# Kernel optimization log

Hardware: AMD Instinct MI355X
Metric: run time of the kernel (lower is better)

Reference implementation:

```python
import jax, jax.numpy as jnp
import numpy as np

B, N, IN_DIM, D = 32, 2000, 3, 5
GROUP = 5
TOPK = 110

def setup_inputs() -> dict:
    key = jax.random.key(0)
    ks = jax.random.split(key, 11)
    def lin(k, fan_in, fan_out):
        kw, kb = jax.random.split(k)
        bound = 1.0 / np.sqrt(fan_in)
        W = jax.random.uniform(kw, (fan_in, fan_out), jnp.float32, -bound, bound)
        b = jax.random.uniform(kb, (fan_out,), jnp.float32, -bound, bound)
        return W, b
    Wi, bi = lin(ks[1], IN_DIM, D)
    Wq, bq = lin(ks[2], D, D)
    Wk, bk = lin(ks[3], D, D)
    Wv, bv = lin(ks[4], D, D)
    Wo, bo = lin(ks[5], D, D)
    in_mat = jax.random.normal(ks[0], (B, N, IN_DIM), jnp.float32)
    return {"in_mat": in_mat, "Wi": Wi, "bi": bi, "Wq": Wq, "bq": bq,
            "Wk": Wk, "bk": bk, "Wv": Wv, "bv": bv, "Wo": Wo, "bo": bo}

def reference(in_mat, Wi, bi, Wq, bq, Wk, bk, Wv, bv, Wo, bo):
    # input projection: [B,N,3] -> [B,N,D]
    x = in_mat @ Wi + bi
    Q = x @ Wq + bq
    K = x @ Wk + bk
    V = x @ Wv + bv
    scores = jnp.einsum('bnd,bmd->bnm', Q, K) / jnp.sqrt(jnp.float32(D))  # [B,N,N]
    attn = jax.nn.softmax(scores, axis=-1)
    context = jnp.einsum('bnm,bmd->bnd', attn, V)
    _out = context @ Wo + bo  # transformed output (unused downstream, as in source)

    # select_points, fully batched
    diag = jnp.diagonal(attn, axis1=1, axis2=2)               # [B,N]
    attn_sums = diag.reshape(B, N // GROUP, GROUP).sum(-1)    # [B, N/5]
    max_group_idx = jnp.argmax(attn_sums, axis=1)             # [B]
    grp_idx = max_group_idx[:, None] * GROUP + jnp.arange(GROUP)[None, :]  # [B,5]
    group_points = jnp.take_along_axis(in_mat, grp_idx[:, :, None], axis=1)  # [B,5,3]
    centroid = group_points.mean(axis=1)                       # [B,3]
    distances = jnp.linalg.norm(in_mat - centroid[:, None, :], axis=-1)  # [B,N]
    _, closest = jax.lax.top_k(-distances, TOPK)               # smallest distances, [B,110]
    selected = jnp.take_along_axis(in_mat, closest[:, :, None], axis=1)  # [B,110,3]
    return selected
```

## Files before the change

### kernel.cpp

```cpp
#include <hip/hip_runtime.h>
#include <stdint.h>

#define BB      32
#define NN      2000
#define TOPK_   110
#define NBIN    2048

__device__ __forceinline__ void fold_weights(
    const float* __restrict__ Wi, const float* __restrict__ bi,
    const float* __restrict__ Wq, const float* __restrict__ bq,
    const float* __restrict__ Wk, const float* __restrict__ bk,
    float Gp[3][3], float vp[3])
{
    const float pf = 0.44721359549995793f * 1.4426950408889634f;
    float Mq[15], Mk[15], cq[5];
#pragma unroll
    for (int d = 0; d < 5; ++d) {
        float s = bq[d];
#pragma unroll
        for (int k = 0; k < 5; ++k) s += bi[k] * Wq[k * 5 + d];
        cq[d] = s;
    }
#pragma unroll
    for (int i = 0; i < 3; ++i)
#pragma unroll
        for (int d = 0; d < 5; ++d) {
            float sq = 0.f, sk = 0.f;
#pragma unroll
            for (int k = 0; k < 5; ++k) {
                sq += Wi[i * 5 + k] * Wq[k * 5 + d];
                sk += Wi[i * 5 + k] * Wk[k * 5 + d];
            }
            Mq[i * 5 + d] = sq;
            Mk[i * 5 + d] = sk;
        }
#pragma unroll
    for (int i = 0; i < 3; ++i)
#pragma unroll
        for (int j = 0; j < 3; ++j) {
            float s = 0.f;
#pragma unroll
            for (int d = 0; d < 5; ++d) s += Mq[i * 5 + d] * Mk[j * 5 + d];
            Gp[i][j] = s * pf;
        }
#pragma unroll
    for (int j = 0; j < 3; ++j) {
        float s = 0.f;
#pragma unroll
        for (int d = 0; d < 5; ++d) s += cq[d] * Mk[j * 5 + d];
        vp[j] = s * pf;
    }
}

__global__ __launch_bounds__(1024) void k_diag(
    const float* __restrict__ in_mat,
    const float* __restrict__ Wi, const float* __restrict__ bi,
    const float* __restrict__ Wq, const float* __restrict__ bq,
    const float* __restrict__ Wk, const float* __restrict__ bk,
    float* __restrict__ diag)
{
    __shared__ float partial[16][128];

    const int b   = blockIdx.y;
    const int rc  = blockIdx.x;
    const int t   = threadIdx.x;
    const int wid = t >> 6;
    const int lane = t & 63;
    const float* inb = in_mat + (size_t)b * NN * 3;

    float Gp[3][3], vp[3];
    fold_weights(Wi, bi, Wq, bq, Wk, bk, Gp, vp);

    float h[2][3];
#pragma unroll
    for (int r = 0; r < 2; ++r) {
        const int row = rc * 128 + r * 64 + lane;
        float p0 = 0.f, p1 = 0.f, p2 = 0.f;
        if (row < NN) {
            p0 = inb[row * 3 + 0];
            p1 = inb[row * 3 + 1];
            p2 = inb[row * 3 + 2];
        }
#pragma unroll
        for (int j = 0; j < 3; ++j)
            h[r][j] = p0 * Gp[0][j] + p1 * Gp[1][j] + p2 * Gp[2][j] + vp[j];
    }

    float acc0 = 0.f, acc1 = 0.f;
    const int m0 = wid * 125;
#pragma unroll 5
    for (int m = m0; m < m0 + 125; ++m) {
        const float px = inb[m * 3 + 0];
        const float py = inb[m * 3 + 1];
        const float pz = inb[m * 3 + 2];
        const float e0 = fmaf(h[0][0], px, fmaf(h[0][1], py, h[0][2] * pz));
        const float e1 = fmaf(h[1][0], px, fmaf(h[1][1], py, h[1][2] * pz));
        acc0 += __builtin_amdgcn_exp2f(e0);
        acc1 += __builtin_amdgcn_exp2f(e1);
    }
    partial[wid][lane]      = acc0;
    partial[wid][64 + lane] = acc1;
    __syncthreads();

    if (t < 128) {
        const int row = rc * 128 + t;
        if (row < NN) {
            float sum = partial[0][t];
#pragma unroll
            for (int w = 1; w < 16; ++w) sum += partial[w][t];
            const float p0 = inb[row * 3 + 0];
            const float p1 = inb[row * 3 + 1];
            const float p2 = inb[row * 3 + 2];
            float hh[3];
#pragma unroll
            for (int j = 0; j < 3; ++j)
                hh[j] = p0 * Gp[0][j] + p1 * Gp[1][j] + p2 * Gp[2][j] + vp[j];
            const float e = fmaf(hh[0], p0, fmaf(hh[1], p1, hh[2] * p2));
            diag[(size_t)b * NN + row] = __builtin_amdgcn_exp2f(e) / sum;
        }
    }
}

__global__ __launch_bounds__(1024) void k_select(
    const float* __restrict__ in_mat,
    const float* __restrict__ diag,
    float* __restrict__ out)
{
    __shared__ unsigned long long keys[2048];
    __shared__ unsigned long long cand[2048];
    __shared__ unsigned int hist[NBIN];
    __shared__ unsigned int sA[NBIN];
    __shared__ unsigned int sB[NBIN];
    __shared__ float        wv[16];
    __shared__ int          wi_[16];
    __shared__ float        centroid[3];
    __shared__ int          thrBin, cnt;

    const int b = blockIdx.x;
    const int t = threadIdx.x;
    const float* dg  = diag + (size_t)b * NN;
    const float* inb = in_mat + (size_t)b * NN * 3;

    hist[t] = 0u; hist[t + 1024] = 0u;
    if (t == 0) cnt = 0;

    float v = -INFINITY; int idx = 0x7fffffff;
    if (t < NN / 5) {
        float s = dg[t * 5 + 0];
        s += dg[t * 5 + 1];
        s += dg[t * 5 + 2];
        s += dg[t * 5 + 3];
        s += dg[t * 5 + 4];
        v = s; idx = t;
    }
#pragma unroll
    for (int off = 32; off > 0; off >>= 1) {
        const float ov = __shfl_down(v, off);
        const int   oi = __shfl_down(idx, off);
        if (ov > v || (ov == v && oi < idx)) { v = ov; idx = oi; }
    }
    if ((t & 63) == 0) { wv[t >> 6] = v; wi_[t >> 6] = idx; }
    __syncthreads();

    if (t == 0) {
        float bv = wv[0]; int bidx = wi_[0];
#pragma unroll
        for (int w = 1; w < 16; ++w) {
            if (wv[w] > bv || (wv[w] == bv && wi_[w] < bidx)) {
                bv = wv[w]; bidx = wi_[w];
            }
        }
        const int base = bidx * 5;
#pragma unroll
        for (int d = 0; d < 3; ++d) {
            float s = inb[(base + 0) * 3 + d];
            s = __fadd_rn(s, inb[(base + 1) * 3 + d]);
            s = __fadd_rn(s, inb[(base + 2) * 3 + d]);
            s = __fadd_rn(s, inb[(base + 3) * 3 + d]);
            s = __fadd_rn(s, inb[(base + 4) * 3 + d]);
            centroid[d] = __fdiv_rn(s, 5.0f);
        }
    }
    __syncthreads();

    const float c0 = centroid[0], c1 = centroid[1], c2 = centroid[2];

#pragma unroll
    for (int r = 0; r < 2; ++r) {
        const int n = r * 1024 + t;
        if (n < NN) {
            const float dx = inb[n * 3 + 0] - c0;
            const float dy = inb[n * 3 + 1] - c1;
            const float dz = inb[n * 3 + 2] - c2;
            const float d2 = __fadd_rn(__fadd_rn(__fmul_rn(dx, dx),
                                                 __fmul_rn(dy, dy)),
                                       __fmul_rn(dz, dz));
            const float dist = __fsqrt_rn(d2);
            const unsigned int db = __float_as_uint(dist);
            keys[n] = ((unsigned long long)db << 32) | (unsigned int)n;
            atomicAdd(&hist[db >> 20], 1u);
        }
    }
    __syncthreads();

    unsigned int* src = hist;
    unsigned int* dst = sA;
    for (int stride = 1; stride < NBIN; stride <<= 1) {
#pragma unroll
        for (int r = 0; r < 2; ++r) {
            const int i = r * 1024 + t;
            dst[i] = src[i] + ((i >= stride) ? src[i - stride] : 0u);
        }
        __syncthreads();
        unsigned int* tmp = (dst == sA) ? sB : sA;
        src = dst; dst = (src == hist) ? sA : tmp;
    }
    const unsigned int* cum = src;

#pragma unroll
    for (int r = 0; r < 2; ++r) {
        const int i = r * 1024 + t;
        if (cum[i] >= TOPK_ && (i == 0 || cum[i - 1] < TOPK_)) thrBin = i;
    }
    __syncthreads();

    const int T = thrBin;
#pragma unroll
    for (int r = 0; r < 2; ++r) {
        const int n = r * 1024 + t;
        if (n < NN) {
            const unsigned long long k = keys[n];
            if ((int)(k >> 52) <= T) {
                const int pos = atomicAdd(&cnt, 1);
                cand[pos] = k;
            }
        }
    }
    __syncthreads();

    const int C = cnt;
    for (int i = t; i < C; i += 1024) {
        const unsigned long long ki = cand[i];
        int rank = 0;
        for (int j = 0; j < C; ++j) rank += (cand[j] < ki);
        if (rank < TOPK_) {
            const int n = (int)(unsigned int)(ki & 0xFFFFFFFFull);
            out[((size_t)b * TOPK_ + rank) * 3 + 0] = inb[n * 3 + 0];
            out[((size_t)b * TOPK_ + rank) * 3 + 1] = inb[n * 3 + 1];
            out[((size_t)b * TOPK_ + rank) * 3 + 2] = inb[n * 3 + 2];
        }
    }
}

extern "C" void kernel_launch(void* const* d_in, const int* in_sizes, int n_in,
                              void* d_out, int out_size, void* d_ws, size_t ws_size,
                              hipStream_t stream) {
    const float* in_mat = (const float*)d_in[0];
    const float* Wi = (const float*)d_in[1];
    const float* bi = (const float*)d_in[2];
    const float* Wq = (const float*)d_in[3];
    const float* bq = (const float*)d_in[4];
    const float* Wk = (const float*)d_in[5];
    const float* bk = (const float*)d_in[6];

    float* diag = (float*)d_ws;
    float* out  = (float*)d_out;

    k_diag<<<dim3(16, BB), 1024, 0, stream>>>(
        in_mat, Wi, bi, Wq, bq, Wk, bk, diag);
    k_select<<<BB, 1024, 0, stream>>>(in_mat, diag, out);
}
```

Baseline: 113.0 us.

## Stage points in LDS, widen row tile to 256, and use wave-shuffle scan

```diff
diff --git a/kernel.cpp b/kernel.cpp
--- a/kernel.cpp
+++ b/kernel.cpp
@@ -59,22 +59,35 @@
     const float* __restrict__ Wk, const float* __restrict__ bk,
     float* __restrict__ diag)
 {
-    __shared__ float partial[16][128];
-
-    const int b   = blockIdx.y;
-    const int rc  = blockIdx.x;
-    const int t   = threadIdx.x;
-    const int wid = t >> 6;
+    __shared__ float xs[2048], ys[2048], zs[2048];
+    __shared__ float partial[16][256];
+
+    const int b    = blockIdx.y;
+    const int rc   = blockIdx.x;
+    const int t    = threadIdx.x;
+    const int wid  = t >> 6;
     const int lane = t & 63;
     const float* inb = in_mat + (size_t)b * NN * 3;
 
     float Gp[3][3], vp[3];
     fold_weights(Wi, bi, Wq, bq, Wk, bk, Gp, vp);
 
-    float h[2][3];
 #pragma unroll
     for (int r = 0; r < 2; ++r) {
-        const int row = rc * 128 + r * 64 + lane;
+        const int n = r * 1024 + t;
+        float p0 = 0.f, p1 = 0.f, p2 = 0.f;
+        if (n < NN) {
+            p0 = inb[n * 3 + 0];
+            p1 = inb[n * 3 + 1];
+            p2 = inb[n * 3 + 2];
+        }
+        xs[n] = p0; ys[n] = p1; zs[n] = p2;
+    }
+
+    float h[4][3];
+#pragma unroll
+    for (int r = 0; r < 4; ++r) {
+        const int row = rc * 256 + r * 64 + lane;
         float p0 = 0.f, p1 = 0.f, p2 = 0.f;
         if (row < NN) {
             p0 = inb[row * 3 + 0];
@@ -85,32 +98,44 @@
         for (int j = 0; j < 3; ++j)
             h[r][j] = p0 * Gp[0][j] + p1 * Gp[1][j] + p2 * Gp[2][j] + vp[j];
     }
-
-    float acc0 = 0.f, acc1 = 0.f;
-    const int m0 = wid * 125;
-#pragma unroll 5
-    for (int m = m0; m < m0 + 125; ++m) {
-        const float px = inb[m * 3 + 0];
-        const float py = inb[m * 3 + 1];
-        const float pz = inb[m * 3 + 2];
-        const float e0 = fmaf(h[0][0], px, fmaf(h[0][1], py, h[0][2] * pz));
-        const float e1 = fmaf(h[1][0], px, fmaf(h[1][1], py, h[1][2] * pz));
-        acc0 += __builtin_amdgcn_exp2f(e0);
-        acc1 += __builtin_amdgcn_exp2f(e1);
-    }
-    partial[wid][lane]      = acc0;
-    partial[wid][64 + lane] = acc1;
-    __syncthreads();
-
-    if (t < 128) {
-        const int row = rc * 128 + t;
+    __syncthreads();
+
+    float acc[4] = {0.f, 0.f, 0.f, 0.f};
+    const int m0 = wid * 128;
+#pragma unroll 2
+    for (int mq = 0; mq < 32; ++mq) {
+        const int m = m0 + mq * 4;
+        const float4 X = *(const float4*)&xs[m];
+        const float4 Y = *(const float4*)&ys[m];
+        const float4 Z = *(const float4*)&zs[m];
+#pragma unroll
+        for (int r = 0; r < 4; ++r) {
+            acc[r] += __builtin_amdgcn_exp2f(
+                fmaf(h[r][0], X.x, fmaf(h[r][1], Y.x, h[r][2] * Z.x)));
+            acc[r] += __builtin_amdgcn_exp2f(
+                fmaf(h[r][0], X.y, fmaf(h[r][1], Y.y, h[r][2] * Z.y)));
+            acc[r] += __builtin_amdgcn_exp2f(
+                fmaf(h[r][0], X.z, fmaf(h[r][1], Y.z, h[r][2] * Z.z)));
+            acc[r] += __builtin_amdgcn_exp2f(
+                fmaf(h[r][0], X.w, fmaf(h[r][1], Y.w, h[r][2] * Z.w)));
+        }
+    }
+    if (wid == 15) {
+#pragma unroll
+        for (int r = 0; r < 4; ++r) acc[r] -= 48.0f;
+    }
+#pragma unroll
+    for (int r = 0; r < 4; ++r)
+        partial[wid][r * 64 + lane] = acc[r];
+    __syncthreads();
+
+    if (t < 256) {
+        const int row = rc * 256 + t;
         if (row < NN) {
             float sum = partial[0][t];
 #pragma unroll
             for (int w = 1; w < 16; ++w) sum += partial[w][t];
-            const float p0 = inb[row * 3 + 0];
-            const float p1 = inb[row * 3 + 1];
-            const float p2 = inb[row * 3 + 2];
+            const float p0 = xs[row], p1 = ys[row], p2 = zs[row];
             float hh[3];
 #pragma unroll
             for (int j = 0; j < 3; ++j)
@@ -129,15 +154,17 @@
     __shared__ unsigned long long keys[2048];
     __shared__ unsigned long long cand[2048];
     __shared__ unsigned int hist[NBIN];
-    __shared__ unsigned int sA[NBIN];
-    __shared__ unsigned int sB[NBIN];
+    __shared__ unsigned int cum[NBIN];
+    __shared__ unsigned int wtot[16];
     __shared__ float        wv[16];
     __shared__ int          wi_[16];
     __shared__ float        centroid[3];
     __shared__ int          thrBin, cnt;
 
-    const int b = blockIdx.x;
-    const int t = threadIdx.x;
+    const int b    = blockIdx.x;
+    const int t    = threadIdx.x;
+    const int wid  = t >> 6;
+    const int lane = t & 63;
     const float* dg  = diag + (size_t)b * NN;
     const float* inb = in_mat + (size_t)b * NN * 3;
 
@@ -159,7 +186,7 @@
         const int   oi = __shfl_down(idx, off);
         if (ov > v || (ov == v && oi < idx)) { v = ov; idx = oi; }
     }
-    if ((t & 63) == 0) { wv[t >> 6] = v; wi_[t >> 6] = idx; }
+    if (lane == 0) { wv[wid] = v; wi_[wid] = idx; }
     __syncthreads();
 
     if (t == 0) {
@@ -203,19 +230,26 @@
     }
     __syncthreads();
 
-    unsigned int* src = hist;
-    unsigned int* dst = sA;
-    for (int stride = 1; stride < NBIN; stride <<= 1) {
-#pragma unroll
-        for (int r = 0; r < 2; ++r) {
-            const int i = r * 1024 + t;
-            dst[i] = src[i] + ((i >= stride) ? src[i - stride] : 0u);
-        }
+    {
+        const int base = wid * 128;
+        unsigned s0 = hist[base + lane];
+        unsigned s1 = hist[base + 64 + lane];
+#pragma unroll
+        for (int off = 1; off < 64; off <<= 1) {
+            const unsigned n0 = __shfl_up(s0, off);
+            const unsigned n1 = __shfl_up(s1, off);
+            if (lane >= off) { s0 += n0; s1 += n1; }
+        }
+        const unsigned t0 = __shfl(s0, 63);
+        s1 += t0;
+        if (lane == 63) wtot[wid] = s1;
         __syncthreads();
-        unsigned int* tmp = (dst == sA) ? sB : sA;
-        src = dst; dst = (src == hist) ? sA : tmp;
-    }
-    const unsigned int* cum = src;
+        unsigned off_ = 0;
+        for (int w = 0; w < wid; ++w) off_ += wtot[w];
+        cum[base + lane]      = s0 + off_;
+        cum[base + 64 + lane] = s1 + off_;
+    }
+    __syncthreads();
 
 #pragma unroll
     for (int r = 0; r < 2; ++r) {
@@ -266,7 +300,7 @@
     float* diag = (float*)d_ws;
     float* out  = (float*)d_out;
 
-    k_diag<<<dim3(16, BB), 1024, 0, stream>>>(
+    k_diag<<<dim3(8, BB), 1024, 0, stream>>>(
         in_mat, Wi, bi, Wq, bq, Wk, bk, diag);
     k_select<<<BB, 1024, 0, stream>>>(in_mat, diag, out);
 }
```

Measured after the change: 106.5 us. 1.06x faster.
